# Optimization experiments

Measured on AMD Instinct MI355X. Metric: run time of the kernel, lower is better.

The kernel has to match this reference:

```python
import jax, jax.numpy as jnp
import numpy as np

TOP_K = 2

def setup_inputs() -> dict:
    key = jax.random.key(0)
    k0, k1, k2, k3 = jax.random.split(key, 4)
    B, S, H, I, E = 2, 2048, 1024, 1408, 8
    hidden_states = jax.random.normal(k0, (B, S, H), dtype=jnp.float32)
    router_weight = jax.random.normal(k1, (E, H), dtype=jnp.float32) * 0.02
    gate_up_proj = jax.random.normal(k2, (E, 2 * I, H), dtype=jnp.float32) * 0.02
    down_proj = jax.random.normal(k3, (E, H, I), dtype=jnp.float32) * 0.02
    return {
        "hidden_states": hidden_states,
        "router_weight": router_weight,
        "gate_up_proj": gate_up_proj,
        "down_proj": down_proj,
    }

def reference(hidden_states, router_weight, gate_up_proj, down_proj):
    B, S, H = hidden_states.shape
    E = router_weight.shape[0]
    x = hidden_states.reshape(-1, H)                       # [T, H]
    T = x.shape[0]
    # Router: logits -> float32 softmax -> top-k (matches torch: topk on probs)
    logits = x @ router_weight.T                           # [T, E]
    probs = jax.nn.softmax(logits.astype(jnp.float32), axis=-1)
    topw, topi = jax.lax.top_k(probs, TOP_K)               # [T, K]
    topw = topw.astype(x.dtype)
    # Per-token combine weights over experts (zero for non-selected experts).
    combine = jnp.zeros((T, E), dtype=x.dtype)
    combine = combine.at[jnp.arange(T)[:, None], topi].set(topw)  # [T, E]
    # Dense grouped expert compute (same math as gather-GEMM-scatter loop:
    # tokens not routed to expert e get combine weight 0).
    gu = jnp.einsum('th,eoh->teo', x, gate_up_proj)        # [T, E, 2I]
    g, u = jnp.split(gu, 2, axis=-1)                       # [T, E, I] each
    h = jax.nn.silu(g) * u                                 # [T, E, I]
    y = jnp.einsum('tei,ehi->teh', h, down_proj)           # [T, E, H]
    out = jnp.einsum('teh,te->th', y, combine)             # [T, H]
    return out.reshape(B, S, H)
```

## Files before the change

### kernel.cpp

```cpp
#include <hip/hip_runtime.h>
#include <math.h>

#define NTOK 4096
#define HDIM 1024
#define NEXP 8
#define IDIM 1408
#define TWO_I 2816
#define BM 128
#define BK 32
#define NRB 72
#define ROWCAP (NRB * BM)

typedef _Float16 f16x8 __attribute__((ext_vector_type(8)));
typedef float f32x4 __attribute__((ext_vector_type(4)));

typedef __attribute__((address_space(1))) const unsigned int gu32;
typedef __attribute__((address_space(3))) unsigned int lu32;
__device__ __forceinline__ void async16(const void* g, void* l) {
  __builtin_amdgcn_global_load_lds((gu32*)g, (lu32*)l, 16, 0, 0);
}

__device__ __forceinline__ void seg_prefix(const int* __restrict__ counts, int* aof) {
  int o = 0; aof[0] = 0;
#pragma unroll
  for (int i = 0; i < 8; i++) { o += (counts[i] + 127) & ~127; aof[i + 1] = o; }
}

extern "C" __global__ void moe_init(int* counts, int* cursor, int* tok) {
  int i = blockIdx.x * 256 + threadIdx.x;
  if (i < NEXP) { counts[i] = 0; cursor[i] = 0; }
  if (i < ROWCAP) tok[i] = -1;
}

#define NG8 (NEXP * TWO_I * HDIM / 8)
#define ND8 (NEXP * HDIM * IDIM / 8)
extern "C" __global__ void moe_cvtw(const float* __restrict__ gup, const float* __restrict__ dp,
                                    _Float16* __restrict__ guph, _Float16* __restrict__ dph) {
  int i = blockIdx.x * 256 + threadIdx.x;
  const float4* s; uint4* d; size_t idx;
  if (i < NG8) { s = (const float4*)gup; d = (uint4*)guph; idx = i; }
  else if (i < NG8 + ND8) { s = (const float4*)dp; d = (uint4*)dph; idx = i - NG8; }
  else return;
  float4 a = s[idx * 2], b = s[idx * 2 + 1];
  union { _Float16 h[8]; uint4 u; } p;
  p.h[0] = (_Float16)a.x; p.h[1] = (_Float16)a.y; p.h[2] = (_Float16)a.z; p.h[3] = (_Float16)a.w;
  p.h[4] = (_Float16)b.x; p.h[5] = (_Float16)b.y; p.h[6] = (_Float16)b.z; p.h[7] = (_Float16)b.w;
  d[idx] = p.u;
}

extern "C" __global__ void moe_router(const float* __restrict__ x,
                                      const float* __restrict__ rw,
                                      int* __restrict__ topi,
                                      float* __restrict__ topw,
                                      _Float16* __restrict__ xh) {
  int w = threadIdx.x >> 6, lane = threadIdx.x & 63;
  int t = blockIdx.x * 4 + w;
  const float4* xp = (const float4*)(x + (size_t)t * HDIM);
  const float4* rp = (const float4*)rw;
  float acc[NEXP];
#pragma unroll
  for (int e = 0; e < NEXP; e++) acc[e] = 0.f;
#pragma unroll
  for (int i = 0; i < HDIM / 256; i++) {
    float4 xv = xp[i * 64 + lane];
    union { _Float16 h[4]; uint2 u; } pk;
    pk.h[0] = (_Float16)xv.x; pk.h[1] = (_Float16)xv.y;
    pk.h[2] = (_Float16)xv.z; pk.h[3] = (_Float16)xv.w;
    *(uint2*)(xh + (size_t)t * HDIM + i * 256 + lane * 4) = pk.u;
#pragma unroll
    for (int e = 0; e < NEXP; e++) {
      float4 rv = rp[e * 256 + i * 64 + lane];
      acc[e] += xv.x * rv.x + xv.y * rv.y + xv.z * rv.z + xv.w * rv.w;
    }
  }
#pragma unroll
  for (int e = 0; e < NEXP; e++) {
#pragma unroll
    for (int off = 32; off > 0; off >>= 1) acc[e] += __shfl_down(acc[e], off);
  }
  if (lane == 0) {
    float m = acc[0];
    for (int e = 1; e < NEXP; e++) m = fmaxf(m, acc[e]);
    float p[NEXP], s = 0.f;
    for (int e = 0; e < NEXP; e++) { p[e] = __expf(acc[e] - m); s += p[e]; }
    float inv = 1.f / s;
    int i0 = 0; float b0 = p[0];
    for (int e = 1; e < NEXP; e++) if (p[e] > b0) { b0 = p[e]; i0 = e; }
    int i1 = -1; float b1 = -1.f;
    for (int e = 0; e < NEXP; e++) if (e != i0 && p[e] > b1) { b1 = p[e]; i1 = e; }
    topi[t * 2] = i0; topi[t * 2 + 1] = i1;
    topw[t * 2] = b0 * inv; topw[t * 2 + 1] = b1 * inv;
  }
}

extern "C" __global__ void moe_count(const int* __restrict__ topi, int* __restrict__ counts) {
  __shared__ int cnt[NEXP];
  if (threadIdx.x < NEXP) cnt[threadIdx.x] = 0;
  __syncthreads();
  int t = blockIdx.x * 256 + threadIdx.x;
  atomicAdd(&cnt[topi[t * 2]], 1);
  atomicAdd(&cnt[topi[t * 2 + 1]], 1);
  __syncthreads();
  if (threadIdx.x < NEXP) atomicAdd(&counts[threadIdx.x], cnt[threadIdx.x]);
}

extern "C" __global__ void moe_scatter(const int* __restrict__ topi, const float* __restrict__ topw,
                                       const int* __restrict__ counts, int* __restrict__ cursor,
                                       int* __restrict__ tok, float* __restrict__ wrow,
                                       int* __restrict__ rows) {
  __shared__ int cnt[NEXP];
  __shared__ int base[NEXP];
  int aof[9]; seg_prefix(counts, aof);
  int tid = threadIdx.x;
  if (tid < NEXP) cnt[tid] = 0;
  __syncthreads();
  int t = blockIdx.x * 256 + tid;
  int e0 = topi[t * 2], e1 = topi[t * 2 + 1];
  int r0 = atomicAdd(&cnt[e0], 1);
  int r1 = atomicAdd(&cnt[e1], 1);
  __syncthreads();
  if (tid < NEXP) base[tid] = atomicAdd(&cursor[tid], cnt[tid]);
  __syncthreads();
  int row0 = aof[e0] + base[e0] + r0;
  int row1 = aof[e1] + base[e1] + r1;
  tok[row0] = t; wrow[row0] = topw[t * 2];     rows[t * 2]     = row0;
  tok[row1] = t; wrow[row1] = topw[t * 2 + 1]; rows[t * 2 + 1] = row1;
}

union SM1 {
  struct { _Float16 a[BM * BK]; _Float16 b[BM * BK]; } st;
  _Float16 ubuf[BM * 66];
};

extern "C" __global__ __launch_bounds__(256) void moe_gemm1(
    const _Float16* __restrict__ xh, const _Float16* __restrict__ guph,
    const int* __restrict__ counts, const int* __restrict__ tok,
    _Float16* __restrict__ hbuf) {
  __shared__ __align__(16) SM1 sm;
  int aof[9]; seg_prefix(counts, aof);
  int fid = blockIdx.x;
  int g = fid & 7, t7 = fid >> 3;
  int jl = t7 % 11, u = t7 / 11;
  int r = u % 9, jh = u / 9;
  int j = jh * 11 + jl;
  int rb = g * 9 + r;
  int row0 = rb * BM;
  if (row0 >= aof[8]) return;
  int e = 0;
#pragma unroll
  for (int i = 0; i < 8; i++) if (row0 >= aof[i]) e = i;

  const int tid = threadIdx.x;
  const int lane = tid & 63, w = tid >> 6;
  const int wm = w & 1, wn = w >> 1;
  const int quad = lane >> 4, l15 = lane & 15;

  f32x4 acc[4][4];
#pragma unroll
  for (int im = 0; im < 4; im++)
#pragma unroll
    for (int in = 0; in < 4; in++) acc[im][in] = (f32x4){0.f, 0.f, 0.f, 0.f};

  const int lq = lane >> 2;
  const int ls = lane & 3;
  const int rA0 = w * 16 + lq, rA1 = rA0 + 64;
  int tA0 = tok[row0 + rA0]; tA0 = tA0 < 0 ? 0 : tA0;
  int tA1 = tok[row0 + rA1]; tA1 = tA1 < 0 ? 0 : tA1;
  const _Float16* gA0 = xh + (size_t)tA0 * HDIM + ls * 8;
  const _Float16* gA1 = xh + (size_t)tA1 * HDIM + ls * 8;
  const _Float16* eb = guph + (size_t)e * TWO_I * HDIM;
  const _Float16* gB0 = eb + (size_t)(j * 64 + rA0) * HDIM + ls * 8;
  const _Float16* gB1 = eb + (size_t)(IDIM + j * 64 + rA0) * HDIM + ls * 8;
  _Float16* lA0 = &sm.st.a[w * 512];
  _Float16* lA1 = &sm.st.a[(w + 4) * 512];
  _Float16* lB0 = &sm.st.b[w * 512];
  _Float16* lB1 = &sm.st.b[(w + 4) * 512];

  for (int kb = 0; kb < HDIM / BK; kb++) {
    async16(gA0, lA0); async16(gA1, lA1);
    async16(gB0, lB0); async16(gB1, lB1);
    gA0 += BK; gA1 += BK; gB0 += BK; gB1 += BK;
    __syncthreads();
    f16x8 av[4], bv[4];
#pragma unroll
    for (int im = 0; im < 4; im++)
      av[im] = *(const f16x8*)&sm.st.a[(wm * 64 + im * 16 + l15) * BK + quad * 8];
#pragma unroll
    for (int in = 0; in < 4; in++)
      bv[in] = *(const f16x8*)&sm.st.b[(wn * 64 + in * 16 + l15) * BK + quad * 8];
#pragma unroll
    for (int im = 0; im < 4; im++)
#pragma unroll
      for (int in = 0; in < 4; in++)
        acc[im][in] = __builtin_amdgcn_mfma_f32_16x16x32_f16(av[im], bv[in], acc[im][in], 0, 0, 0);
    __syncthreads();
  }

  if (wn == 1) {
#pragma unroll
    for (int im = 0; im < 4; im++)
#pragma unroll
      for (int in = 0; in < 4; in++)
#pragma unroll
        for (int r2 = 0; r2 < 4; r2++)
          sm.ubuf[(wm * 64 + im * 16 + quad * 4 + r2) * 66 + in * 16 + l15] = (_Float16)acc[im][in][r2];
  }
  __syncthreads();
  if (wn == 0) {
#pragma unroll
    for (int im = 0; im < 4; im++)
#pragma unroll
      for (int in = 0; in < 4; in++)
#pragma unroll
        for (int r2 = 0; r2 < 4; r2++) {
          float gg = acc[im][in][r2];
          float uu = (float)sm.ubuf[(wm * 64 + im * 16 + quad * 4 + r2) * 66 + in * 16 + l15];
          float hh = gg / (1.f + __expf(-gg)) * uu;
          int row = row0 + wm * 64 + im * 16 + quad * 4 + r2;
          hbuf[(size_t)row * IDIM + j * 64 + in * 16 + l15] = (_Float16)hh;
        }
  }
}

extern "C" __global__ __launch_bounds__(256) void moe_gemm2(
    const _Float16* __restrict__ hbuf, const _Float16* __restrict__ dph,
    const int* __restrict__ counts, const float* __restrict__ wrow,
    _Float16* __restrict__ yh) {
  __shared__ __align__(16) struct { _Float16 a[BM * BK]; _Float16 b[BM * BK]; } sm;
  int aof[9]; seg_prefix(counts, aof);
  int fid = blockIdx.x;
  int g = fid & 7, t7 = fid >> 3;
  int cb = t7 & 7, r = t7 >> 3;
  int rb = g * 9 + r;
  int row0 = rb * BM;
  if (row0 >= aof[8]) return;
  int e = 0;
#pragma unroll
  for (int i = 0; i < 8; i++) if (row0 >= aof[i]) e = i;

  const int tid = threadIdx.x;
  const int lane = tid & 63, w = tid >> 6;
  const int wm = w & 1, wn = w >> 1;
  const int quad = lane >> 4, l15 = lane & 15;

  f32x4 acc[4][4];
#pragma unroll
  for (int im = 0; im < 4; im++)
#pragma unroll
    for (int in = 0; in < 4; in++) acc[im][in] = (f32x4){0.f, 0.f, 0.f, 0.f};

  const int lq = lane >> 2, ls = lane & 3;
  const int rA0 = w * 16 + lq;
  const _Float16* gA0 = hbuf + (size_t)(row0 + rA0) * IDIM + ls * 8;
  const _Float16* gA1 = gA0 + (size_t)64 * IDIM;
  const _Float16* eb = dph + (size_t)e * HDIM * IDIM;
  const _Float16* gB0 = eb + (size_t)(cb * 128 + rA0) * IDIM + ls * 8;
  const _Float16* gB1 = gB0 + (size_t)64 * IDIM;
  _Float16* lA0 = &sm.a[w * 512];
  _Float16* lA1 = &sm.a[(w + 4) * 512];
  _Float16* lB0 = &sm.b[w * 512];
  _Float16* lB1 = &sm.b[(w + 4) * 512];

  for (int kb = 0; kb < IDIM / BK; kb++) {
    async16(gA0, lA0); async16(gA1, lA1);
    async16(gB0, lB0); async16(gB1, lB1);
    gA0 += BK; gA1 += BK; gB0 += BK; gB1 += BK;
    __syncthreads();
    f16x8 av[4], bv[4];
#pragma unroll
    for (int im = 0; im < 4; im++)
      av[im] = *(const f16x8*)&sm.a[(wm * 64 + im * 16 + l15) * BK + quad * 8];
#pragma unroll
    for (int in = 0; in < 4; in++)
      bv[in] = *(const f16x8*)&sm.b[(wn * 64 + in * 16 + l15) * BK + quad * 8];
#pragma unroll
    for (int im = 0; im < 4; im++)
#pragma unroll
      for (int in = 0; in < 4; in++)
        acc[im][in] = __builtin_amdgcn_mfma_f32_16x16x32_f16(av[im], bv[in], acc[im][in], 0, 0, 0);
    __syncthreads();
  }

#pragma unroll
  for (int im = 0; im < 4; im++) {
#pragma unroll
    for (int r2 = 0; r2 < 4; r2++) {
      int row = row0 + wm * 64 + im * 16 + quad * 4 + r2;
      float wgt = wrow[row];
#pragma unroll
      for (int in = 0; in < 4; in++) {
        int col = cb * 128 + wn * 64 + in * 16 + l15;
        yh[(size_t)row * HDIM + col] = (_Float16)(acc[im][in][r2] * wgt);
      }
    }
  }
}

extern "C" __global__ void moe_combine(const _Float16* __restrict__ yh,
                                       const int* __restrict__ rows,
                                       float* __restrict__ out) {
  int i = blockIdx.x * 256 + threadIdx.x;
  int t = i >> 7, c8 = i & 127;
  int rA = rows[t * 2], rB = rows[t * 2 + 1];
  union { uint4 u; _Float16 h[8]; } pa, pb;
  pa.u = ((const uint4*)(yh + (size_t)rA * HDIM))[c8];
  pb.u = ((const uint4*)(yh + (size_t)rB * HDIM))[c8];
  float4 o0, o1;
  o0.x = (float)pa.h[0] + (float)pb.h[0]; o0.y = (float)pa.h[1] + (float)pb.h[1];
  o0.z = (float)pa.h[2] + (float)pb.h[2]; o0.w = (float)pa.h[3] + (float)pb.h[3];
  o1.x = (float)pa.h[4] + (float)pb.h[4]; o1.y = (float)pa.h[5] + (float)pb.h[5];
  o1.z = (float)pa.h[6] + (float)pb.h[6]; o1.w = (float)pa.h[7] + (float)pb.h[7];
  ((float4*)out)[(size_t)i * 2] = o0;
  ((float4*)out)[(size_t)i * 2 + 1] = o1;
}

extern "C" void kernel_launch(void* const* d_in, const int* in_sizes, int n_in,
                              void* d_out, int out_size, void* d_ws, size_t ws_size,
                              hipStream_t stream) {
  const float* x   = (const float*)d_in[0];
  const float* rw  = (const float*)d_in[1];
  const float* gup = (const float*)d_in[2];
  const float* dp  = (const float*)d_in[3];
  float* out = (float*)d_out;

  char* ws = (char*)d_ws;
  int*   counts = (int*)ws;
  int*   cursor = (int*)(ws + 64);
  int*   topi   = (int*)(ws + 4096);
  float* topw   = (float*)(ws + 36864);
  int*   tok    = (int*)(ws + 69632);
  float* wrow   = (float*)(ws + 106496);
  int*   rows   = (int*)(ws + 143360);
  _Float16* xh   = (_Float16*)(ws + 176128);
  _Float16* guph = (_Float16*)(ws + 8564736);
  _Float16* dph  = (_Float16*)(ws + 54702080);
  _Float16* hbuf = (_Float16*)(ws + 77770752);
  _Float16* yh   = (_Float16*)(ws + 103723008);

  moe_init<<<(ROWCAP + 255) / 256, 256, 0, stream>>>(counts, cursor, tok);
  moe_router<<<NTOK / 4, 256, 0, stream>>>(x, rw, topi, topw, xh);
  moe_count<<<NTOK / 256, 256, 0, stream>>>(topi, counts);
  moe_scatter<<<NTOK / 256, 256, 0, stream>>>(topi, topw, counts, cursor, tok, wrow, rows);
  moe_cvtw<<<(NG8 + ND8 + 255) / 256, 256, 0, stream>>>(gup, dp, guph, dph);
  moe_gemm1<<<8 * 22 * 9, 256, 0, stream>>>(xh, guph, counts, tok, hbuf);
  moe_gemm2<<<8 * 8 * 9, 256, 0, stream>>>(hbuf, dph, counts, wrow, yh);
  moe_combine<<<NTOK * HDIM / 8 / 256, 256, 0, stream>>>(yh, rows, out);
}
```

Measured before the change: 336.4 us.

## Rewrite grouped GEMMs with 256x256 tiles, swizzled LDS and double-buffered pipeline

Both expert GEMMs move from 128x128x32 tiles with 256 threads to 256-row tiles with TK=64 and 512 threads. Global-to-LDS loads are double-buffered and prefetched two k-steps ahead, interleaved with MFMA phases under barriers and s_setprio. LDS uses an XOR swizzle to avoid bank conflicts, and expert segments are padded to 256 rows. The aim is higher MFMA utilization and fewer LDS and global reloads per flop. The cost is more padding waste per expert, fewer blocks in flight, and yh now aliases the guph buffer, which is dead after gemm1.

```diff
diff --git a/kernel.cpp b/kernel.cpp
--- a/kernel.cpp
+++ b/kernel.cpp
@@ -6,10 +6,10 @@
 #define NEXP 8
 #define IDIM 1408
 #define TWO_I 2816
-#define BM 128
-#define BK 32
-#define NRB 72
-#define ROWCAP (NRB * BM)
+#define TM 256
+#define TK 64
+#define NRB 40
+#define ROWCAP (NRB * 256)
 
 typedef _Float16 f16x8 __attribute__((ext_vector_type(8)));
 typedef float f32x4 __attribute__((ext_vector_type(4)));
@@ -23,7 +23,7 @@
 __device__ __forceinline__ void seg_prefix(const int* __restrict__ counts, int* aof) {
   int o = 0; aof[0] = 0;
 #pragma unroll
-  for (int i = 0; i < 8; i++) { o += (counts[i] + 127) & ~127; aof[i + 1] = o; }
+  for (int i = 0; i < 8; i++) { o += (counts[i] + 255) & ~255; aof[i + 1] = o; }
 }
 
 extern "C" __global__ void moe_init(int* counts, int* cursor, int* tok) {
@@ -127,171 +127,187 @@
   tok[row1] = t; wrow[row1] = topw[t * 2 + 1]; rows[t * 2 + 1] = row1;
 }
 
-union SM1 {
-  struct { _Float16 a[BM * BK]; _Float16 b[BM * BK]; } st;
-  _Float16 ubuf[BM * 66];
-};
-
-extern "C" __global__ __launch_bounds__(256) void moe_gemm1(
+
+#define DSR(dst, a) asm volatile("ds_read_b128 %0, %1" : "=v"(dst) : "v"(a))
+#define WAITLGKM() { asm volatile("s_waitcnt lgkmcnt(0)" ::: "memory"); __builtin_amdgcn_sched_barrier(0); }
+#define WAITVM(n) asm volatile("s_waitcnt vmcnt(" #n ")" ::: "memory")
+#define BAR() __builtin_amdgcn_s_barrier()
+#define PRIO(x) __builtin_amdgcn_s_setprio(x)
+
+#define RD_A(grp, BO) { \
+  _Pragma("unroll") for (int m_ = 0; m_ < 4; m_++) { \
+    DSR(va[m_][0], sA0 + (BO) + ((grp)*4 + m_)*2048); \
+    DSR(va[m_][1], sA1 + (BO) + ((grp)*4 + m_)*2048); } }
+
+#define RD_B(VB, nb, BO) { \
+  _Pragma("unroll") for (int n_ = 0; n_ < 2; n_++) { \
+    DSR(VB[n_][0], sB0 + (BO) + ((nb)*2 + n_)*2048); \
+    DSR(VB[n_][1], sB1 + (BO) + ((nb)*2 + n_)*2048); } }
+
+#define MM(qa, qb, VB) { \
+  _Pragma("unroll") for (int k_ = 0; k_ < 2; k_++) \
+  _Pragma("unroll") for (int m_ = 0; m_ < 4; m_++) \
+  _Pragma("unroll") for (int n_ = 0; n_ < 2; n_++) \
+    acc[(qa)*4 + m_][(qb)*2 + n_] = __builtin_amdgcn_mfma_f32_16x16x32_f16( \
+        va[m_][k_], VB[n_][k_], acc[(qa)*4 + m_][(qb)*2 + n_], 0, 0, 0); }
+
+#define STG4(P, bf, r0, kt) { \
+  async16(P[0][0] + (kt)*TK, smem + ((bf)*4 + (r0))*8192 + wv*512); \
+  async16(P[0][1] + (kt)*TK, smem + ((bf)*4 + (r0))*8192 + 4096 + wv*512); \
+  async16(P[1][0] + (kt)*TK, smem + ((bf)*4 + (r0) + 1)*8192 + wv*512); \
+  async16(P[1][1] + (kt)*TK, smem + ((bf)*4 + (r0) + 1)*8192 + 4096 + wv*512); }
+#define STAGE_A(bf, kt) STG4(pA, bf, 0, kt)
+#define STAGE_B(bf, kt) STG4(pB, bf, 2, kt)
+
+#define GEMM_CORE(NIT) { \
+  STAGE_B(0, 0); STAGE_A(0, 0); \
+  STAGE_B(1, 1); STAGE_A(1, 1); \
+  WAITVM(8); BAR(); \
+  _Pragma("unroll 1") \
+  for (int it = 0; it < (NIT); ++it) { \
+    const int nl = (it + 1 < (NIT)); \
+    const int kt2 = 2*it + 2, kt3 = 2*it + 3; \
+     RD_A(0, 0); RD_B(vb0, 0, 0); BAR(); WAITLGKM(); PRIO(1); MM(0,0,vb0); PRIO(0); BAR(); \
+     RD_B(vb1, 1, 0); BAR(); WAITLGKM(); PRIO(1); MM(0,1,vb1); PRIO(0); BAR(); \
+     RD_A(1, 0); if (nl) STAGE_B(0, kt2); BAR(); WAITLGKM(); PRIO(1); MM(1,0,vb0); PRIO(0); BAR(); \
+     if (nl) { STAGE_A(0, kt2); } PRIO(1); MM(1,1,vb1); PRIO(0); \
+              if (nl) { WAITVM(8); } else { WAITVM(0); } BAR(); \
+     RD_A(0, 65536); RD_B(vb0, 0, 65536); BAR(); WAITLGKM(); PRIO(1); MM(0,0,vb0); PRIO(0); BAR(); \
+     RD_B(vb1, 1, 65536); BAR(); WAITLGKM(); PRIO(1); MM(0,1,vb1); PRIO(0); BAR(); \
+     RD_A(1, 65536); if (nl) STAGE_B(1, kt3); BAR(); WAITLGKM(); PRIO(1); MM(1,0,vb0); PRIO(0); BAR(); \
+     if (nl) { STAGE_A(1, kt3); } PRIO(1); MM(1,1,vb1); PRIO(0); \
+              if (nl) { WAITVM(8); } BAR(); \
+  } \
+  asm volatile("" ::: "memory"); }
+
+#define GEMM_SETUP() \
+  const int tid = threadIdx.x; \
+  const int lane = tid & 63, wv = tid >> 6; \
+  const int wm = wv >> 2, wn = wv & 3; \
+  const int quad = lane >> 4, l15 = lane & 15; \
+  const int srow = tid >> 3; \
+  const int kc = ((tid & 7) ^ (srow & 7)) << 3; \
+  const uint32_t lb = (uint32_t)(uintptr_t)&smem[0]; \
+  const uint32_t c0 = (uint32_t)((quad * 16) ^ ((l15 & 7) << 4)); \
+  const uint32_t c1 = c0 ^ 64; \
+  const uint32_t sA0 = lb + wm * 16384 + l15 * 128 + c0; \
+  const uint32_t sA1 = lb + wm * 16384 + l15 * 128 + c1; \
+  const uint32_t sB0 = lb + (2 + (wn >> 1)) * 16384 + ((wn & 1) * 64 + l15) * 128 + c0; \
+  const uint32_t sB1 = lb + (2 + (wn >> 1)) * 16384 + ((wn & 1) * 64 + l15) * 128 + c1; \
+  f32x4 acc[8][4]; \
+  _Pragma("unroll") for (int m = 0; m < 8; m++) \
+  _Pragma("unroll") for (int n = 0; n < 4; n++) acc[m][n] = (f32x4){0.f, 0.f, 0.f, 0.f}; \
+  f16x8 va[4][2], vb0[2][2], vb1[2][2];
+
+extern "C" __global__ __launch_bounds__(512, 2) void moe_gemm1(
     const _Float16* __restrict__ xh, const _Float16* __restrict__ guph,
     const int* __restrict__ counts, const int* __restrict__ tok,
     _Float16* __restrict__ hbuf) {
-  __shared__ __align__(16) SM1 sm;
+  __shared__ __align__(128) _Float16 smem[65536];
   int aof[9]; seg_prefix(counts, aof);
-  int fid = blockIdx.x;
-  int g = fid & 7, t7 = fid >> 3;
-  int jl = t7 % 11, u = t7 / 11;
-  int r = u % 9, jh = u / 9;
-  int j = jh * 11 + jl;
-  int rb = g * 9 + r;
-  int row0 = rb * BM;
+  const int fid = blockIdx.x;
+  const int g = fid & 7, t7 = fid >> 3;
+  const int j = t7 / 5, r5 = t7 - j * 5;
+  const int rb = g + 8 * r5;
+  const int row0 = rb * TM;
   if (row0 >= aof[8]) return;
   int e = 0;
 #pragma unroll
   for (int i = 0; i < 8; i++) if (row0 >= aof[i]) e = i;
 
-  const int tid = threadIdx.x;
-  const int lane = tid & 63, w = tid >> 6;
-  const int wm = w & 1, wn = w >> 1;
-  const int quad = lane >> 4, l15 = lane & 15;
-
-  f32x4 acc[4][4];
-#pragma unroll
-  for (int im = 0; im < 4; im++)
-#pragma unroll
-    for (int in = 0; in < 4; in++) acc[im][in] = (f32x4){0.f, 0.f, 0.f, 0.f};
-
-  const int lq = lane >> 2;
-  const int ls = lane & 3;
-  const int rA0 = w * 16 + lq, rA1 = rA0 + 64;
-  int tA0 = tok[row0 + rA0]; tA0 = tA0 < 0 ? 0 : tA0;
-  int tA1 = tok[row0 + rA1]; tA1 = tA1 < 0 ? 0 : tA1;
-  const _Float16* gA0 = xh + (size_t)tA0 * HDIM + ls * 8;
-  const _Float16* gA1 = xh + (size_t)tA1 * HDIM + ls * 8;
+  GEMM_SETUP();
+
+  const _Float16* pA[2][2]; const _Float16* pB[2][2];
+#pragma unroll
+  for (int h = 0; h < 2; h++)
+#pragma unroll
+    for (int q = 0; q < 2; q++) {
+      int tk = tok[row0 + h * 128 + q * 64 + srow];
+      tk = tk < 0 ? 0 : tk;
+      pA[h][q] = xh + (size_t)tk * HDIM + kc;
+    }
   const _Float16* eb = guph + (size_t)e * TWO_I * HDIM;
-  const _Float16* gB0 = eb + (size_t)(j * 64 + rA0) * HDIM + ls * 8;
-  const _Float16* gB1 = eb + (size_t)(IDIM + j * 64 + rA0) * HDIM + ls * 8;
-  _Float16* lA0 = &sm.st.a[w * 512];
-  _Float16* lA1 = &sm.st.a[(w + 4) * 512];
-  _Float16* lB0 = &sm.st.b[w * 512];
-  _Float16* lB1 = &sm.st.b[(w + 4) * 512];
-
-  for (int kb = 0; kb < HDIM / BK; kb++) {
-    async16(gA0, lA0); async16(gA1, lA1);
-    async16(gB0, lB0); async16(gB1, lB1);
-    gA0 += BK; gA1 += BK; gB0 += BK; gB1 += BK;
-    __syncthreads();
-    f16x8 av[4], bv[4];
-#pragma unroll
-    for (int im = 0; im < 4; im++)
-      av[im] = *(const f16x8*)&sm.st.a[(wm * 64 + im * 16 + l15) * BK + quad * 8];
-#pragma unroll
-    for (int in = 0; in < 4; in++)
-      bv[in] = *(const f16x8*)&sm.st.b[(wn * 64 + in * 16 + l15) * BK + quad * 8];
-#pragma unroll
-    for (int im = 0; im < 4; im++)
-#pragma unroll
-      for (int in = 0; in < 4; in++)
-        acc[im][in] = __builtin_amdgcn_mfma_f32_16x16x32_f16(av[im], bv[in], acc[im][in], 0, 0, 0);
-    __syncthreads();
-  }
-
-  if (wn == 1) {
-#pragma unroll
-    for (int im = 0; im < 4; im++)
-#pragma unroll
-      for (int in = 0; in < 4; in++)
+#pragma unroll
+  for (int q = 0; q < 2; q++) {
+    pB[0][q] = eb + (size_t)(j * 128 + q * 64 + srow) * HDIM + kc;
+    pB[1][q] = eb + (size_t)(IDIM + j * 128 + q * 64 + srow) * HDIM + kc;
+  }
+
+  GEMM_CORE(HDIM / (2 * TK))
+
+  if (wn >= 2) {
+#pragma unroll
+    for (int mf = 0; mf < 8; mf++)
+#pragma unroll
+      for (int nf = 0; nf < 4; nf++)
 #pragma unroll
         for (int r2 = 0; r2 < 4; r2++)
-          sm.ubuf[(wm * 64 + im * 16 + quad * 4 + r2) * 66 + in * 16 + l15] = (_Float16)acc[im][in][r2];
-  }
-  __syncthreads();
-  if (wn == 0) {
-#pragma unroll
-    for (int im = 0; im < 4; im++)
-#pragma unroll
-      for (int in = 0; in < 4; in++)
-#pragma unroll
-        for (int r2 = 0; r2 < 4; r2++) {
-          float gg = acc[im][in][r2];
-          float uu = (float)sm.ubuf[(wm * 64 + im * 16 + quad * 4 + r2) * 66 + in * 16 + l15];
+          smem[(wm * 128 + mf * 16 + quad * 4 + r2) * 132 + (wn - 2) * 64 + nf * 16 + l15] =
+              (_Float16)acc[mf][nf][r2];
+  }
+  __syncthreads();
+  if (wn < 2) {
+#pragma unroll
+    for (int mf = 0; mf < 8; mf++) {
+#pragma unroll
+      for (int r2 = 0; r2 < 4; r2++) {
+        const int rl = wm * 128 + mf * 16 + quad * 4 + r2;
+        _Float16* orow = hbuf + (size_t)(row0 + rl) * IDIM + j * 128 + wn * 64;
+#pragma unroll
+        for (int nf = 0; nf < 4; nf++) {
+          float gg = acc[mf][nf][r2];
+          float uu = (float)smem[rl * 132 + wn * 64 + nf * 16 + l15];
           float hh = gg / (1.f + __expf(-gg)) * uu;
-          int row = row0 + wm * 64 + im * 16 + quad * 4 + r2;
-          hbuf[(size_t)row * IDIM + j * 64 + in * 16 + l15] = (_Float16)hh;
+          orow[nf * 16 + l15] = (_Float16)hh;
         }
-  }
-}
-
-extern "C" __global__ __launch_bounds__(256) void moe_gemm2(
+      }
+    }
+  }
+}
+
+extern "C" __global__ __launch_bounds__(512, 2) void moe_gemm2(
     const _Float16* __restrict__ hbuf, const _Float16* __restrict__ dph,
     const int* __restrict__ counts, const float* __restrict__ wrow,
     _Float16* __restrict__ yh) {
-  __shared__ __align__(16) struct { _Float16 a[BM * BK]; _Float16 b[BM * BK]; } sm;
+  __shared__ __align__(128) _Float16 smem[65536];
   int aof[9]; seg_prefix(counts, aof);
-  int fid = blockIdx.x;
-  int g = fid & 7, t7 = fid >> 3;
-  int cb = t7 & 7, r = t7 >> 3;
-  int rb = g * 9 + r;
-  int row0 = rb * BM;
+  const int fid = blockIdx.x;
+  const int g = fid & 7, t7 = fid >> 3;
+  const int cb = t7 / 5, r5 = t7 - cb * 5;
+  const int rb = g + 8 * r5;
+  const int row0 = rb * TM;
   if (row0 >= aof[8]) return;
   int e = 0;
 #pragma unroll
   for (int i = 0; i < 8; i++) if (row0 >= aof[i]) e = i;
 
-  const int tid = threadIdx.x;
-  const int lane = tid & 63, w = tid >> 6;
-  const int wm = w & 1, wn = w >> 1;
-  const int quad = lane >> 4, l15 = lane & 15;
-
-  f32x4 acc[4][4];
-#pragma unroll
-  for (int im = 0; im < 4; im++)
-#pragma unroll
-    for (int in = 0; in < 4; in++) acc[im][in] = (f32x4){0.f, 0.f, 0.f, 0.f};
-
-  const int lq = lane >> 2, ls = lane & 3;
-  const int rA0 = w * 16 + lq;
-  const _Float16* gA0 = hbuf + (size_t)(row0 + rA0) * IDIM + ls * 8;
-  const _Float16* gA1 = gA0 + (size_t)64 * IDIM;
+  GEMM_SETUP();
+
+  const _Float16* pA[2][2]; const _Float16* pB[2][2];
+#pragma unroll
+  for (int h = 0; h < 2; h++)
+#pragma unroll
+    for (int q = 0; q < 2; q++)
+      pA[h][q] = hbuf + (size_t)(row0 + h * 128 + q * 64 + srow) * IDIM + kc;
   const _Float16* eb = dph + (size_t)e * HDIM * IDIM;
-  const _Float16* gB0 = eb + (size_t)(cb * 128 + rA0) * IDIM + ls * 8;
-  const _Float16* gB1 = gB0 + (size_t)64 * IDIM;
-  _Float16* lA0 = &sm.a[w * 512];
-  _Float16* lA1 = &sm.a[(w + 4) * 512];
-  _Float16* lB0 = &sm.b[w * 512];
-  _Float16* lB1 = &sm.b[(w + 4) * 512];
-
-  for (int kb = 0; kb < IDIM / BK; kb++) {
-    async16(gA0, lA0); async16(gA1, lA1);
-    async16(gB0, lB0); async16(gB1, lB1);
-    gA0 += BK; gA1 += BK; gB0 += BK; gB1 += BK;
-    __syncthreads();
-    f16x8 av[4], bv[4];
-#pragma unroll
-    for (int im = 0; im < 4; im++)
-      av[im] = *(const f16x8*)&sm.a[(wm * 64 + im * 16 + l15) * BK + quad * 8];
-#pragma unroll
-    for (int in = 0; in < 4; in++)
-      bv[in] = *(const f16x8*)&sm.b[(wn * 64 + in * 16 + l15) * BK + quad * 8];
-#pragma unroll
-    for (int im = 0; im < 4; im++)
-#pragma unroll
-      for (int in = 0; in < 4; in++)
-        acc[im][in] = __builtin_amdgcn_mfma_f32_16x16x32_f16(av[im], bv[in], acc[im][in], 0, 0, 0);
-    __syncthreads();
-  }
-
-#pragma unroll
-  for (int im = 0; im < 4; im++) {
+#pragma unroll
+  for (int h = 0; h < 2; h++)
+#pragma unroll
+    for (int q = 0; q < 2; q++)
+      pB[h][q] = eb + (size_t)(cb * 256 + h * 128 + q * 64 + srow) * IDIM + kc;
+
+  GEMM_CORE(IDIM / (2 * TK))
+
+#pragma unroll
+  for (int mf = 0; mf < 8; mf++) {
 #pragma unroll
     for (int r2 = 0; r2 < 4; r2++) {
-      int row = row0 + wm * 64 + im * 16 + quad * 4 + r2;
-      float wgt = wrow[row];
-#pragma unroll
-      for (int in = 0; in < 4; in++) {
-        int col = cb * 128 + wn * 64 + in * 16 + l15;
-        yh[(size_t)row * HDIM + col] = (_Float16)(acc[im][in][r2] * wgt);
-      }
+      const int row = row0 + wm * 128 + mf * 16 + quad * 4 + r2;
+      const float wgt = wrow[row];
+      _Float16* orow = yh + (size_t)row * HDIM + cb * 256 + wn * 64;
+#pragma unroll
+      for (int nf = 0; nf < 4; nf++)
+        orow[nf * 16 + l15] = (_Float16)(acc[mf][nf][r2] * wgt);
     }
   }
 }
@@ -329,20 +345,20 @@
   int*   topi   = (int*)(ws + 4096);
   float* topw   = (float*)(ws + 36864);
   int*   tok    = (int*)(ws + 69632);
-  float* wrow   = (float*)(ws + 106496);
-  int*   rows   = (int*)(ws + 143360);
-  _Float16* xh   = (_Float16*)(ws + 176128);
-  _Float16* guph = (_Float16*)(ws + 8564736);
-  _Float16* dph  = (_Float16*)(ws + 54702080);
-  _Float16* hbuf = (_Float16*)(ws + 77770752);
-  _Float16* yh   = (_Float16*)(ws + 103723008);
+  float* wrow   = (float*)(ws + 110592);
+  int*   rows   = (int*)(ws + 151552);
+  _Float16* xh   = (_Float16*)(ws + 184320);
+  _Float16* guph = (_Float16*)(ws + 8572928);
+  _Float16* dph  = (_Float16*)(ws + 54710272);
+  _Float16* hbuf = (_Float16*)(ws + 77778944);
+  _Float16* yh   = (_Float16*)(ws + 8572928);
 
   moe_init<<<(ROWCAP + 255) / 256, 256, 0, stream>>>(counts, cursor, tok);
   moe_router<<<NTOK / 4, 256, 0, stream>>>(x, rw, topi, topw, xh);
   moe_count<<<NTOK / 256, 256, 0, stream>>>(topi, counts);
   moe_scatter<<<NTOK / 256, 256, 0, stream>>>(topi, topw, counts, cursor, tok, wrow, rows);
   moe_cvtw<<<(NG8 + ND8 + 255) / 256, 256, 0, stream>>>(gup, dp, guph, dph);
-  moe_gemm1<<<8 * 22 * 9, 256, 0, stream>>>(xh, guph, counts, tok, hbuf);
-  moe_gemm2<<<8 * 8 * 9, 256, 0, stream>>>(hbuf, dph, counts, wrow, yh);
+  moe_gemm1<<<8 * 11 * 5, 512, 0, stream>>>(xh, guph, counts, tok, hbuf);
+  moe_gemm2<<<8 * 4 * 5, 512, 0, stream>>>(hbuf, dph, counts, wrow, yh);
   moe_combine<<<NTOK * HDIM / 8 / 256, 256, 0, stream>>>(yh, rows, out);
 }
```

Result: no change. 331.2 us (-1.6%).
